# Optimization experiments

Hardware: AMD Instinct MI355X
Metric: run time of the kernel (lower is better)

## Reference

```python
import jax, jax.numpy as jnp
import numpy as np

IN_BW = 4
W_BW = 4
EPS = 1e-5


def quantize(x, bw):
    # k-bit uniform quantizer on [-1, 1 - 2^(1-bw)] with straight-through rounding
    scale = 2.0 ** (bw - 1)
    xc = jnp.clip(x, -1.0, 1.0 - 1.0 / scale)
    q = jnp.round(xc * scale) / scale
    return xc + jax.lax.stop_gradient(q - xc)


def bconv(x, w, stride):
    # BinarizeConv2d: quantize activations (in_bw) and weights (weight_bw), then conv
    return jax.lax.conv_general_dilated(
        quantize(x, IN_BW), quantize(w, W_BW),
        window_strides=stride, padding='VALID',
        dimension_numbers=('NCHW', 'OIHW', 'NCHW'))


def bn2d(x, g, b):
    mean = x.mean(axis=(0, 2, 3), keepdims=True)
    var = x.var(axis=(0, 2, 3), keepdims=True)
    return (x - mean) * jax.lax.rsqrt(var + EPS) * g.reshape(1, -1, 1, 1) + b.reshape(1, -1, 1, 1)


def bn1d(x, g, b):
    mean = x.mean(axis=0, keepdims=True)
    var = x.var(axis=0, keepdims=True)
    return (x - mean) * jax.lax.rsqrt(var + EPS) * g + b


def htanh(x):
    return jnp.clip(x, -1.0, 1.0)


def setup_inputs() -> dict:
    key = jax.random.key(0)
    ks = jax.random.split(key, 24)
    B = 8192
    d = {'x': jax.random.normal(ks[0], (B, 1, 1250, 1), dtype=jnp.float32)}
    # conv weights OIHW
    shapes = [(3, 1, 6, 1), (5, 3, 5, 1), (10, 5, 4, 1), (20, 10, 4, 1), (20, 20, 4, 1)]
    for i, s in enumerate(shapes):
        d[f'w{i+1}'] = 0.3 * jax.random.normal(ks[1 + i], s, dtype=jnp.float32)
    d['fw1'] = 0.3 * jax.random.normal(ks[6], (10, 740), dtype=jnp.float32)
    d['fw2'] = 0.3 * jax.random.normal(ks[7], (2, 10), dtype=jnp.float32)
    chans = [3, 5, 10, 20, 20, 10, 2]
    for i, c in enumerate(chans):
        d[f'g{i+1}'] = 1.0 + 0.1 * jax.random.normal(ks[8 + i], (c,), dtype=jnp.float32)
        d[f'b{i+1}'] = 0.1 * jax.random.normal(ks[15 + i], (c,), dtype=jnp.float32)
    return d


def reference(x, w1, w2, w3, w4, w5, fw1, fw2,
              g1, g2, g3, g4, g5, g6, g7,
              b1, b2, b3, b4, b5, b6, b7):
    h = htanh(bn2d(bconv(x, w1, (2, 1)), g1, b1))
    h = htanh(bn2d(bconv(h, w2, (2, 1)), g2, b2))
    h = htanh(bn2d(bconv(h, w3, (2, 1)), g3, b3))
    h = htanh(bn2d(bconv(h, w4, (2, 1)), g4, b4))
    h = htanh(bn2d(bconv(h, w5, (2, 1)), g5, b5))
    h = h.reshape(h.shape[0], -1)  # (B, 20*37*1) = (B, 740)
    # dropout is identity in eval mode
    h = htanh(bn1d(quantize(h, IN_BW) @ quantize(fw1, W_BW).T, g6, b6))
    h = bn1d(quantize(h, IN_BW) @ quantize(fw2, W_BW).T, g7, b7)
    return h
```

## Files before the change

kernel.cpp:

```cpp
#include <hip/hip_runtime.h>

#define DEV __device__ __forceinline__

DEV float qwt(float w) {
    float y = fminf(fmaxf(w, -1.0f), 0.875f);
    return rintf(y * 8.0f) * 0.125f;
}
DEV int qw8i(float w) {
    float y = fminf(fmaxf(w, -1.0f), 0.875f);
    return (int)rintf(y * 8.0f);
}
DEV int q8i(float x, float a, float b) {
    float y = fmaf(x, a, b);
    y = fminf(fmaxf(y, -1.0f), 0.875f);
    return (int)rintf(y * 8.0f);
}
DEV float qact(float x, float a, float b) {
    float y = fmaf(x, a, b);
    y = fminf(fmaxf(y, -1.0f), 0.875f);
    return rintf(y * 8.0f) * 0.125f;
}

DEV int dot4(int a, int b, int c) {
#if __has_builtin(__builtin_amdgcn_sdot4)
    return __builtin_amdgcn_sdot4(a, b, c, false);
#else
    c += (int)(signed char)(a)       * (int)(signed char)(b);
    c += (int)(signed char)(a >> 8)  * (int)(signed char)(b >> 8);
    c += (int)(signed char)(a >> 16) * (int)(signed char)(b >> 16);
    c += (int)(signed char)(a >> 24) * (int)(signed char)(b >> 24);
    return c;
#endif
}
DEV unsigned alignpair(unsigned hi, unsigned lo, int bits) {
#if __has_builtin(__builtin_amdgcn_alignbit)
    return __builtin_amdgcn_alignbit(hi, lo, bits);
#else
    return bits ? ((lo >> bits) | (hi << (32 - bits))) : lo;
#endif
}

DEV void pack_layer(const float* w, int* o, int CIN, int COUT, int K, int t) {
    int KW = (K + 3) / 4;
    for (int i = t; i < COUT * CIN * KW; i += 256) {
        int j = i % KW, cc = i / KW;
        unsigned r = 0;
        for (int u = 0; u < 4; u++) {
            int k = 4 * j + u;
            int b = (k < K) ? (qw8i(w[cc * K + k]) & 0xff) : 0;
            r |= (unsigned)b << (8 * u);
        }
        o[i] = (int)r;
    }
}
__global__ __launch_bounds__(256) void pack_k(
    const float* w1, const float* w2, const float* w3, const float* w4, const float* w5,
    int* o1, int* o2, int* o3, int* o4, int* o5)
{
    int t = threadIdx.x;
    pack_layer(w1, o1, 1, 3, 6, t);
    pack_layer(w2, o2, 3, 5, 5, t);
    pack_layer(w3, o3, 5, 10, 4, t);
    pack_layer(w4, o4, 10, 20, 4, t);
    pack_layer(w5, o5, 20, 20, 4, t);
}

template<int CIN,int COUT,int K,int LINP,int LOUT,int LOUTP,int P,int R,bool IN_FLOAT,int LIN=0>
__global__ __launch_bounds__(256) void conv_k(
    const void* __restrict__ in_, const int* __restrict__ wqi,
    const float* __restrict__ tr, short* __restrict__ out,
    float* __restrict__ partial, int B)
{
    constexpr int KW   = (K + 3) / 4;
    constexpr int NE   = P + 2 * KW - 2 + 1;
    constexpr int ND   = (2 * (NE - 1) + 3) / 4 + 2;
    constexpr int LO_P = (LOUT + P - 1) / P;
    constexpr int GROUPS = R * LO_P;

    __shared__ __align__(16) signed char smem[R * CIN * LINP + 32];
    __shared__ float ts[CIN > 0 ? CIN : 1], tb[CIN > 0 ? CIN : 1];
    __shared__ float red[4][2 * COUT];

    const int tid = threadIdx.x;

    if constexpr (!IN_FLOAT) {
        if (tid < CIN) {
            ts[tid] = tr[tid] * 0.015625f;
            tb[tid] = tr[CIN + tid];
        }
        __syncthreads();
    }

    const int r0   = blockIdx.x * R;
    const int rcnt = min(R, B - r0);

    if constexpr (IN_FLOAT) {
        constexpr int CH = LIN / 2;
        const float2* gp = (const float2*)in_;
        for (int c = tid; c < rcnt * CH; c += 256) {
            int r = c / CH, rem = c - r * CH;
            float2 v = gp[(size_t)(r0 + r) * CH + rem];
            int b0 = q8i(v.x, 1.f, 0.f) & 0xff;
            int b1 = q8i(v.y, 1.f, 0.f) & 0xff;
            *(unsigned short*)(smem + r * LINP + rem * 2) =
                (unsigned short)(b0 | (b1 << 8));
        }
    } else {
        constexpr int CH  = CIN * LINP / 8;
        constexpr int CHC = LINP / 8;
        const int4* gp = (const int4*)((const short*)in_ + (size_t)r0 * CIN * LINP);
        for (int c = tid; c < rcnt * CH; c += 256) {
            int rem = c % CH;
            int ci = rem / CHC;
            float a = ts[ci], bo = tb[ci];
            int4 v = gp[c];
            int vs[4] = { v.x, v.y, v.z, v.w };
            unsigned pk[2];
#pragma unroll
            for (int u = 0; u < 2; u++) {
                unsigned pp = 0;
#pragma unroll
                for (int j = 0; j < 2; j++) {
                    int word = vs[u * 2 + j];
                    int b0 = q8i((float)(short)(word & 0xffff), a, bo) & 0xff;
                    int b1 = q8i((float)(short)(word >> 16),    a, bo) & 0xff;
                    pp |= (unsigned)(b0 | (b1 << 8)) << (16 * j);
                }
                pk[u] = pp;
            }
            ((uint2*)smem)[c] = make_uint2(pk[0], pk[1]);
        }
    }
    __syncthreads();

    float tsum[COUT], tsq[COUT];
#pragma unroll
    for (int c = 0; c < COUT; c++) { tsum[c] = 0.f; tsq[c] = 0.f; }

#pragma unroll 1
    for (int g = tid; g < GROUPS; g += 256) {
        int r = g / LO_P;
        if (r >= rcnt) continue;
        int l0   = (g - r * LO_P) * P;
        int pact = min(P, LOUT - l0);

        int acc[COUT][P];
#pragma unroll
        for (int co = 0; co < COUT; co++)
#pragma unroll
            for (int p = 0; p < P; p++) acc[co][p] = 0;

        const int ibase = r * CIN * LINP + 2 * l0;
        const int sh    = (P % 2 == 0) ? 0 : (ibase & 3);

        for (int ci = 0; ci < CIN; ci++) {
            const int* sp = (const int*)smem + ((ci * LINP + (ibase & ~3)) >> 2);
            int d[ND];
#pragma unroll
            for (int j = 0; j < ND; j++) d[j] = sp[j];
            int e[NE];
#pragma unroll
            for (int i = 0; i < NE; i++) {
                int off = sh + 2 * i;
                e[i] = (int)alignpair((unsigned)d[off / 4 + 1], (unsigned)d[off / 4], (off & 3) * 8);
            }
#pragma unroll
            for (int co = 0; co < COUT; co++) {
#pragma unroll
                for (int j = 0; j < KW; j++) {
                    int wv = wqi[(co * CIN + ci) * KW + j];
#pragma unroll
                    for (int p = 0; p < P; p++)
                        acc[co][p] = dot4(e[p + 2 * j], wv, acc[co][p]);
                }
            }
        }

        const size_t ob = (size_t)(r0 + r) * COUT * LOUTP + l0;
#pragma unroll
        for (int co = 0; co < COUT; co++) {
            if (pact == P) {
                short tmp[P];
#pragma unroll
                for (int p = 0; p < P; p++) {
                    tmp[p] = (short)acc[co][p];
                    float v = (float)acc[co][p] * 0.015625f;
                    tsum[co] += v;
                    tsq[co]   = fmaf(v, v, tsq[co]);
                }
                short* op = &out[ob + (size_t)co * LOUTP];
                if constexpr (P == 1) {
                    op[0] = tmp[0];
                } else if constexpr (P == 2) {
                    *(short2*)op = make_short2(tmp[0], tmp[1]);
                } else if constexpr (P == 4) {
                    *(short4*)op = make_short4(tmp[0], tmp[1], tmp[2], tmp[3]);
                } else if constexpr (P == 8) {
                    *(short4*)op       = make_short4(tmp[0], tmp[1], tmp[2], tmp[3]);
                    *(short4*)(op + 4) = make_short4(tmp[4], tmp[5], tmp[6], tmp[7]);
                }
            } else {
#pragma unroll
                for (int p = 0; p < P; p++) {
                    if (p < pact) {
                        out[ob + (size_t)co * LOUTP + p] = (short)acc[co][p];
                        float v = (float)acc[co][p] * 0.015625f;
                        tsum[co] += v;
                        tsq[co]   = fmaf(v, v, tsq[co]);
                    }
                }
            }
        }
    }

    const int lane = tid & 63, wid = tid >> 6;
#pragma unroll
    for (int co = 0; co < COUT; co++) {
        float s = tsum[co], q = tsq[co];
        for (int off = 32; off > 0; off >>= 1) {
            s += __shfl_down(s, off, 64);
            q += __shfl_down(q, off, 64);
        }
        if (lane == 0) { red[wid][2 * co] = s; red[wid][2 * co + 1] = q; }
    }
    __syncthreads();
    if (tid < 2 * COUT) {
        float v = red[0][tid] + red[1][tid] + red[2][tid] + red[3][tid];
        partial[(size_t)blockIdx.x * (2 * COUT) + tid] = v;
    }
}

__global__ __launch_bounds__(256) void finalize_k(
    const float* __restrict__ partial, int G, int C, double N,
    const float* __restrict__ gamma, const float* __restrict__ beta,
    float* __restrict__ trout)
{
    const int c = blockIdx.x;
    double s = 0.0, q = 0.0;
    for (int g = threadIdx.x; g < G; g += 256) {
        s += (double)partial[(size_t)g * 2 * C + 2 * c];
        q += (double)partial[(size_t)g * 2 * C + 2 * c + 1];
    }
    for (int off = 32; off > 0; off >>= 1) {
        s += __shfl_down(s, off, 64);
        q += __shfl_down(q, off, 64);
    }
    __shared__ double rs[4], rq[4];
    int lane = threadIdx.x & 63, wid = threadIdx.x >> 6;
    if (lane == 0) { rs[wid] = s; rq[wid] = q; }
    __syncthreads();
    if (threadIdx.x == 0) {
        double S = rs[0] + rs[1] + rs[2] + rs[3];
        double Q = rq[0] + rq[1] + rq[2] + rq[3];
        double mean = S / N;
        double var  = Q / N - mean * mean;
        double inv  = 1.0 / sqrt(var + 1e-5);
        double sc   = (double)gamma[c] * inv;
        trout[c]     = (float)sc;
        trout[C + c] = (float)((double)beta[c] - mean * sc);
    }
}

__global__ __launch_bounds__(256) void fc1_k(
    const short* __restrict__ y5, const float* __restrict__ fw1,
    const float* __restrict__ tr, float* __restrict__ z1,
    float* __restrict__ partial, int B)
{
    __shared__ float wq[7400];
    __shared__ float ts[20], tb[20];
    __shared__ float red[4][20];
    const int tid = threadIdx.x;
    for (int i = tid; i < 7400; i += 256) wq[i] = qwt(fw1[i]);
    if (tid < 20) { ts[tid] = tr[tid]; tb[tid] = tr[20 + tid]; }
    __syncthreads();

    const int lane = tid & 63, wid = tid >> 6;
    float tsum[10], tsq[10];
#pragma unroll
    for (int j = 0; j < 10; j++) { tsum[j] = 0.f; tsq[j] = 0.f; }

#pragma unroll 1
    for (int r = blockIdx.x * 4 + wid; r < B; r += gridDim.x * 4) {
        const short* xr = y5 + (size_t)r * 800;
        float acc[10];
#pragma unroll
        for (int j = 0; j < 10; j++) acc[j] = 0.f;
#pragma unroll 1
        for (int f = lane; f < 740; f += 64) {
            int c = f / 37, pos = f - c * 37;
            float x = qact((float)xr[c * 40 + pos] * 0.015625f, ts[c], tb[c]);
#pragma unroll
            for (int j = 0; j < 10; j++) acc[j] = fmaf(x, wq[j * 740 + f], acc[j]);
        }
#pragma unroll
        for (int j = 0; j < 10; j++) {
            float v = acc[j];
            for (int off = 1; off < 64; off <<= 1) v += __shfl_xor(v, off, 64);
            tsum[j] += v; tsq[j] = fmaf(v, v, tsq[j]);
            if (lane == j) z1[(size_t)r * 10 + j] = v;
        }
    }
    if (lane == 0) {
#pragma unroll
        for (int j = 0; j < 10; j++) { red[wid][2 * j] = tsum[j]; red[wid][2 * j + 1] = tsq[j]; }
    }
    __syncthreads();
    if (tid < 20) {
        float v = red[0][tid] + red[1][tid] + red[2][tid] + red[3][tid];
        partial[(size_t)blockIdx.x * 20 + tid] = v;
    }
}

__global__ __launch_bounds__(256) void fc2_fused_k(
    const float* __restrict__ z1, const float* __restrict__ fw2,
    const float* __restrict__ part6, int G6,
    const float* __restrict__ g6, const float* __restrict__ b6,
    const float* __restrict__ g7, const float* __restrict__ b7,
    float* __restrict__ outp, int B)
{
    __shared__ float zbuf[16384];
    __shared__ double dred[4][20];
    __shared__ double dtot[20];
    __shared__ float ts7[10], tb7[10], wq2[20];
    __shared__ float fr[4][4];
    __shared__ float tr8[4];

    const int tid = threadIdx.x;
    const int lane = tid & 63, wid = tid >> 6;

    double ls[20];
#pragma unroll
    for (int c = 0; c < 20; c++) ls[c] = 0.0;
    for (int g = tid; g < G6; g += 256) {
#pragma unroll
        for (int c = 0; c < 20; c++) ls[c] += (double)part6[(size_t)g * 20 + c];
    }
#pragma unroll
    for (int c = 0; c < 20; c++) {
        double v = ls[c];
        for (int off = 32; off > 0; off >>= 1) v += __shfl_down(v, off, 64);
        if (lane == 0) dred[wid][c] = v;
    }
    if (tid < 20) wq2[tid] = qwt(fw2[tid]);
    __syncthreads();
    if (tid < 20) dtot[tid] = dred[0][tid] + dred[1][tid] + dred[2][tid] + dred[3][tid];
    __syncthreads();
    if (tid < 10) {
        double N = (double)B;
        double mean = dtot[2 * tid] / N;
        double var  = dtot[2 * tid + 1] / N - mean * mean;
        double inv  = 1.0 / sqrt(var + 1e-5);
        double sc   = (double)g6[tid] * inv;
        ts7[tid] = (float)sc;
        tb7[tid] = (float)((double)b6[tid] - mean * sc);
    }
    __syncthreads();

    float s0 = 0.f, q0 = 0.f, s1 = 0.f, q1 = 0.f;
#pragma unroll 1
    for (int r = tid; r < B; r += 256) {
        float a0 = 0.f, a1 = 0.f;
#pragma unroll
        for (int i = 0; i < 10; i++) {
            float x = qact(z1[(size_t)r * 10 + i], ts7[i], tb7[i]);
            a0 = fmaf(x, wq2[i], a0);
            a1 = fmaf(x, wq2[10 + i], a1);
        }
        zbuf[r * 2]     = a0;
        zbuf[r * 2 + 1] = a1;
        s0 += a0; q0 = fmaf(a0, a0, q0);
        s1 += a1; q1 = fmaf(a1, a1, q1);
    }
    for (int off = 32; off > 0; off >>= 1) {
        s0 += __shfl_down(s0, off, 64); q0 += __shfl_down(q0, off, 64);
        s1 += __shfl_down(s1, off, 64); q1 += __shfl_down(q1, off, 64);
    }
    if (lane == 0) { fr[wid][0] = s0; fr[wid][1] = q0; fr[wid][2] = s1; fr[wid][3] = q1; }
    __syncthreads();
    if (tid < 2) {
        double S = 0.0, Q = 0.0;
        for (int w = 0; w < 4; w++) { S += (double)fr[w][2 * tid]; Q += (double)fr[w][2 * tid + 1]; }
        double N = (double)B;
        double mean = S / N;
        double var  = Q / N - mean * mean;
        double inv  = 1.0 / sqrt(var + 1e-5);
        double sc   = (double)g7[tid] * inv;
        tr8[tid]     = (float)sc;
        tr8[2 + tid] = (float)((double)b7[tid] - mean * sc);
    }
    __syncthreads();
    for (int i = tid; i < 2 * B; i += 256) {
        int c = i & 1;
        outp[i] = fmaf(zbuf[i], tr8[c], tr8[2 + c]);
    }
}

extern "C" void kernel_launch(void* const* d_in, const int* in_sizes, int n_in,
                              void* d_out, int out_size, void* d_ws, size_t ws_size,
                              hipStream_t stream)
{
    const float* x   = (const float*)d_in[0];
    const float* w1  = (const float*)d_in[1];
    const float* w2  = (const float*)d_in[2];
    const float* w3  = (const float*)d_in[3];
    const float* w4  = (const float*)d_in[4];
    const float* w5  = (const float*)d_in[5];
    const float* fw1 = (const float*)d_in[6];
    const float* fw2 = (const float*)d_in[7];
    const float *g[7], *bb[7];
    for (int i = 0; i < 7; i++) { g[i] = (const float*)d_in[8 + 2 * i]; bb[i] = (const float*)d_in[9 + 2 * i]; }

    char* ws = (char*)d_ws;
    size_t off = 0;
    auto alloc = [&](size_t bytes) -> void* {
        void* p = ws + off;
        off += (bytes + 255) & ~(size_t)255;
        return p;
    };
    short* SA      = (short*)alloc((size_t)8192 * 3 * 624 * 2);
    short* SB      = (short*)alloc((size_t)8192 * 20 * 80 * 2);
    float* z1      = (float*)alloc((size_t)81920 * 4);
    float* partial = (float*)alloc((size_t)81920 * 4);
    int*   wp1 = (int*)alloc(64);   int* wp2 = (int*)alloc(256);
    int*   wp3 = (int*)alloc(256);  int* wp4 = (int*)alloc(1024);
    int*   wp5 = (int*)alloc(2048);
    float* tr2 = (float*)alloc(256); float* tr3 = (float*)alloc(256);
    float* tr4 = (float*)alloc(256); float* tr5 = (float*)alloc(256);
    float* tr6 = (float*)alloc(256);

    const int B = 8192;

    pack_k<<<1, 256, 0, stream>>>(w1, w2, w3, w4, w5, wp1, wp2, wp3, wp4, wp5);

    {
        int grid = (B + 2) / 3;
        conv_k<1, 3, 6, 1252, 623, 624, 8, 3, true, 1250>
            <<<grid, 256, 0, stream>>>(x, wp1, nullptr, SA, partial, B);
        finalize_k<<<3, 256, 0, stream>>>(partial, grid, 3, (double)B * 623.0, g[0], bb[0], tr2);
    }
    {
        int grid = (B + 5) / 6;
        conv_k<3, 5, 5, 624, 310, 312, 8, 6, false>
            <<<grid, 256, 0, stream>>>(SA, wp2, tr2, SB, partial, B);
        finalize_k<<<5, 256, 0, stream>>>(partial, grid, 5, (double)B * 310.0, g[1], bb[1], tr3);
    }
    {
        int grid = (B + 5) / 6;
        conv_k<5, 10, 4, 312, 154, 160, 4, 6, false>
            <<<grid, 256, 0, stream>>>(SB, wp3, tr3, SA, partial, B);
        finalize_k<<<10, 256, 0, stream>>>(partial, grid, 10, (double)B * 154.0, g[2], bb[2], tr4);
    }
    {
        int grid = (B + 6) / 7;
        conv_k<10, 20, 4, 160, 76, 80, 2, 7, false>
            <<<grid, 256, 0, stream>>>(SA, wp4, tr4, SB, partial, B);
        finalize_k<<<20, 256, 0, stream>>>(partial, grid, 20, (double)B * 76.0, g[3], bb[3], tr5);
    }
    {
        int grid = (B + 6) / 7;
        conv_k<20, 20, 4, 80, 37, 40, 1, 7, false>
            <<<grid, 256, 0, stream>>>(SB, wp5, tr5, SA, partial, B);
        finalize_k<<<20, 256, 0, stream>>>(partial, grid, 20, (double)B * 37.0, g[4], bb[4], tr6);
    }
    {
        int grid = 512;
        fc1_k<<<grid, 256, 0, stream>>>(SA, fw1, tr6, z1, partial, B);
    }
    fc2_fused_k<<<1, 256, 0, stream>>>(z1, fw2, partial, 512,
                                       g[5], bb[5], g[6], bb[6],
                                       (float*)d_out, B);
}
```

Before: 305.8 us.

## Fuse the whole network into one persistent cooperative kernel with grid syncs

Replaces the chain of per-layer conv, finalize, fc1 and fc2 kernels with a single cooperative persistent kernel. Layers are separated by grid.sync(), and each block recomputes the batch-norm scale and shift from the partial sums. Each block processes 16-row tiles in a grid-stride loop, and weight packing is done per block in LDS. This removes roughly a dozen kernel launches and the serial single-block tail, at the cost of grid-wide barriers, fixed occupancy limits (512 or 256 blocks) and redundant per-block reduction work.

```diff
diff --git a/kernel.cpp b/kernel.cpp
--- a/kernel.cpp
+++ b/kernel.cpp
@@ -1,4 +1,7 @@
 #include <hip/hip_runtime.h>
+#include <hip/hip_cooperative_groups.h>
+
+namespace cg = cooperative_groups;
 
 #define DEV __device__ __forceinline__
 
@@ -40,173 +43,187 @@
 #endif
 }
 
-DEV void pack_layer(const float* w, int* o, int CIN, int COUT, int K, int t) {
-    int KW = (K + 3) / 4;
-    for (int i = t; i < COUT * CIN * KW; i += 256) {
+struct Params {
+    const float* x;
+    const float* w1; const float* w2; const float* w3; const float* w4; const float* w5;
+    const float* fw1; const float* fw2;
+    const float* g[7]; const float* bb[7];
+    short* y1; short* y2; short* y3; short* y4; short* y5;
+    float* z1; float* z2;
+    float* part[7];
+    float* out;
+    int G;
+};
+
+template<int C>
+DEV void bridge(const float* part, int G, double N,
+                const float* gamma, const float* beta,
+                float* tsA, float* tbA, float fold, double* dsc)
+{
+    const int tid = threadIdx.x;
+    if (tid < 2 * C * 4) {
+        int slot = tid >> 2, ch = tid & 3;
+        double s = 0.0;
+        for (int g = ch; g < G; g += 4)
+            s += (double)part[(size_t)g * 2 * C + slot];
+        dsc[tid] = s;
+    }
+    __syncthreads();
+    if (tid < C) {
+        double S = dsc[8 * tid]     + dsc[8 * tid + 1] + dsc[8 * tid + 2] + dsc[8 * tid + 3];
+        double Q = dsc[8 * tid + 4] + dsc[8 * tid + 5] + dsc[8 * tid + 6] + dsc[8 * tid + 7];
+        double mean = S / N;
+        double var  = Q / N - mean * mean;
+        double inv  = 1.0 / sqrt(var + 1e-5);
+        double sc   = (double)gamma[tid] * inv;
+        tsA[tid] = (float)sc * fold;
+        tbA[tid] = (float)((double)beta[tid] - mean * sc);
+    }
+    __syncthreads();
+}
+
+template<int CIN,int COUT,int K,int LINP,int LOUT,int LOUTP,int P,bool IN_FLOAT,int LIN>
+DEV void conv_layer(const void* in_, const float* w, short* out, float* partial,
+                    int G, signed char* uni, int* wql,
+                    const float* tsA, const float* tbA, float (*redf)[40])
+{
+    constexpr int KW   = (K + 3) / 4;
+    constexpr int NE   = P + 2 * KW - 1;
+    constexpr int ND   = (2 * (NE - 1) + 3) / 4 + 2;
+    constexpr int LO_P = (LOUT + P - 1) / P;
+    constexpr int GROUPS = 16 * LO_P;
+
+    const int tid = threadIdx.x;
+    const int bid = blockIdx.x;
+
+    for (int i = tid; i < COUT * CIN * KW; i += 256) {
         int j = i % KW, cc = i / KW;
-        unsigned r = 0;
+        unsigned rr = 0;
         for (int u = 0; u < 4; u++) {
             int k = 4 * j + u;
-            int b = (k < K) ? (qw8i(w[cc * K + k]) & 0xff) : 0;
-            r |= (unsigned)b << (8 * u);
-        }
-        o[i] = (int)r;
-    }
-}
-__global__ __launch_bounds__(256) void pack_k(
-    const float* w1, const float* w2, const float* w3, const float* w4, const float* w5,
-    int* o1, int* o2, int* o3, int* o4, int* o5)
-{
-    int t = threadIdx.x;
-    pack_layer(w1, o1, 1, 3, 6, t);
-    pack_layer(w2, o2, 3, 5, 5, t);
-    pack_layer(w3, o3, 5, 10, 4, t);
-    pack_layer(w4, o4, 10, 20, 4, t);
-    pack_layer(w5, o5, 20, 20, 4, t);
-}
-
-template<int CIN,int COUT,int K,int LINP,int LOUT,int LOUTP,int P,int R,bool IN_FLOAT,int LIN=0>
-__global__ __launch_bounds__(256) void conv_k(
-    const void* __restrict__ in_, const int* __restrict__ wqi,
-    const float* __restrict__ tr, short* __restrict__ out,
-    float* __restrict__ partial, int B)
-{
-    constexpr int KW   = (K + 3) / 4;
-    constexpr int NE   = P + 2 * KW - 2 + 1;
-    constexpr int ND   = (2 * (NE - 1) + 3) / 4 + 2;
-    constexpr int LO_P = (LOUT + P - 1) / P;
-    constexpr int GROUPS = R * LO_P;
-
-    __shared__ __align__(16) signed char smem[R * CIN * LINP + 32];
-    __shared__ float ts[CIN > 0 ? CIN : 1], tb[CIN > 0 ? CIN : 1];
-    __shared__ float red[4][2 * COUT];
-
-    const int tid = threadIdx.x;
-
-    if constexpr (!IN_FLOAT) {
-        if (tid < CIN) {
-            ts[tid] = tr[tid] * 0.015625f;
-            tb[tid] = tr[CIN + tid];
-        }
+            int bv = (k < K) ? (qw8i(w[cc * K + k]) & 0xff) : 0;
+            rr |= (unsigned)bv << (8 * u);
+        }
+        wql[i] = (int)rr;
+    }
+
+    float tsum[COUT], tsq[COUT];
+#pragma unroll
+    for (int c = 0; c < COUT; c++) { tsum[c] = 0.f; tsq[c] = 0.f; }
+
+    for (int tile = bid; tile < 512; tile += G) {
+        const int r0 = tile * 16;
         __syncthreads();
-    }
-
-    const int r0   = blockIdx.x * R;
-    const int rcnt = min(R, B - r0);
-
-    if constexpr (IN_FLOAT) {
-        constexpr int CH = LIN / 2;
-        const float2* gp = (const float2*)in_;
-        for (int c = tid; c < rcnt * CH; c += 256) {
-            int r = c / CH, rem = c - r * CH;
-            float2 v = gp[(size_t)(r0 + r) * CH + rem];
-            int b0 = q8i(v.x, 1.f, 0.f) & 0xff;
-            int b1 = q8i(v.y, 1.f, 0.f) & 0xff;
-            *(unsigned short*)(smem + r * LINP + rem * 2) =
-                (unsigned short)(b0 | (b1 << 8));
-        }
-    } else {
-        constexpr int CH  = CIN * LINP / 8;
-        constexpr int CHC = LINP / 8;
-        const int4* gp = (const int4*)((const short*)in_ + (size_t)r0 * CIN * LINP);
-        for (int c = tid; c < rcnt * CH; c += 256) {
-            int rem = c % CH;
-            int ci = rem / CHC;
-            float a = ts[ci], bo = tb[ci];
-            int4 v = gp[c];
-            int vs[4] = { v.x, v.y, v.z, v.w };
-            unsigned pk[2];
-#pragma unroll
-            for (int u = 0; u < 2; u++) {
-                unsigned pp = 0;
-#pragma unroll
-                for (int j = 0; j < 2; j++) {
-                    int word = vs[u * 2 + j];
-                    int b0 = q8i((float)(short)(word & 0xffff), a, bo) & 0xff;
-                    int b1 = q8i((float)(short)(word >> 16),    a, bo) & 0xff;
-                    pp |= (unsigned)(b0 | (b1 << 8)) << (16 * j);
+
+        if constexpr (IN_FLOAT) {
+            constexpr int CH = LIN / 2;
+            const float2* gp = (const float2*)in_;
+            for (int c = tid; c < 16 * CH; c += 256) {
+                int r = c / CH, rem = c - r * CH;
+                float2 v = gp[(size_t)(r0 + r) * CH + rem];
+                int b0 = q8i(v.x, 1.f, 0.f) & 0xff;
+                int b1 = q8i(v.y, 1.f, 0.f) & 0xff;
+                *(unsigned short*)(uni + r * LINP + rem * 2) =
+                    (unsigned short)(b0 | (b1 << 8));
+            }
+        } else {
+            constexpr int CH  = CIN * LINP / 8;
+            constexpr int CHC = LINP / 8;
+            const int4* gp = (const int4*)((const short*)in_ + (size_t)r0 * CIN * LINP);
+            for (int c = tid; c < 16 * CH; c += 256) {
+                int rem = c % CH;
+                int ci = rem / CHC;
+                float a = tsA[ci], bo = tbA[ci];
+                int4 v = gp[c];
+                int vs[4] = { v.x, v.y, v.z, v.w };
+                unsigned pk[2];
+#pragma unroll
+                for (int u = 0; u < 2; u++) {
+                    unsigned pp = 0;
+#pragma unroll
+                    for (int j = 0; j < 2; j++) {
+                        int word = vs[u * 2 + j];
+                        int b0 = q8i((float)(short)(word & 0xffff), a, bo) & 0xff;
+                        int b1 = q8i((float)(short)(word >> 16),    a, bo) & 0xff;
+                        pp |= (unsigned)(b0 | (b1 << 8)) << (16 * j);
+                    }
+                    pk[u] = pp;
                 }
-                pk[u] = pp;
-            }
-            ((uint2*)smem)[c] = make_uint2(pk[0], pk[1]);
-        }
-    }
-    __syncthreads();
-
-    float tsum[COUT], tsq[COUT];
-#pragma unroll
-    for (int c = 0; c < COUT; c++) { tsum[c] = 0.f; tsq[c] = 0.f; }
+                ((uint2*)uni)[c] = make_uint2(pk[0], pk[1]);
+            }
+        }
+        __syncthreads();
 
 #pragma unroll 1
-    for (int g = tid; g < GROUPS; g += 256) {
-        int r = g / LO_P;
-        if (r >= rcnt) continue;
-        int l0   = (g - r * LO_P) * P;
-        int pact = min(P, LOUT - l0);
-
-        int acc[COUT][P];
-#pragma unroll
-        for (int co = 0; co < COUT; co++)
-#pragma unroll
-            for (int p = 0; p < P; p++) acc[co][p] = 0;
-
-        const int ibase = r * CIN * LINP + 2 * l0;
-        const int sh    = (P % 2 == 0) ? 0 : (ibase & 3);
-
-        for (int ci = 0; ci < CIN; ci++) {
-            const int* sp = (const int*)smem + ((ci * LINP + (ibase & ~3)) >> 2);
-            int d[ND];
-#pragma unroll
-            for (int j = 0; j < ND; j++) d[j] = sp[j];
-            int e[NE];
-#pragma unroll
-            for (int i = 0; i < NE; i++) {
-                int off = sh + 2 * i;
-                e[i] = (int)alignpair((unsigned)d[off / 4 + 1], (unsigned)d[off / 4], (off & 3) * 8);
-            }
+        for (int g = tid; g < GROUPS; g += 256) {
+            int r = g / LO_P;
+            int l0   = (g - r * LO_P) * P;
+            int pact = min(P, LOUT - l0);
+
+            int acc[COUT][P];
+#pragma unroll
+            for (int co = 0; co < COUT; co++)
+#pragma unroll
+                for (int p = 0; p < P; p++) acc[co][p] = 0;
+
+            const int ibase = r * CIN * LINP + 2 * l0;
+            const int sh    = (P % 2 == 0) ? 0 : (ibase & 3);
+
+            for (int ci = 0; ci < CIN; ci++) {
+                const int* sp = (const int*)uni + ((ci * LINP + (ibase & ~3)) >> 2);
+                int d[ND];
+#pragma unroll
+                for (int j = 0; j < ND; j++) d[j] = sp[j];
+                int e[NE];
+#pragma unroll
+                for (int i = 0; i < NE; i++) {
+                    int off = sh + 2 * i;
+                    e[i] = (int)alignpair((unsigned)d[off / 4 + 1], (unsigned)d[off / 4], (off & 3) * 8);
+                }
+#pragma unroll
+                for (int co = 0; co < COUT; co++) {
+#pragma unroll
+                    for (int j = 0; j < KW; j++) {
+                        int wv = wql[(co * CIN + ci) * KW + j];
+#pragma unroll
+                        for (int p = 0; p < P; p++)
+                            acc[co][p] = dot4(e[p + 2 * j], wv, acc[co][p]);
+                    }
+                }
+            }
+
+            const size_t ob = (size_t)(r0 + r) * COUT * LOUTP + l0;
 #pragma unroll
             for (int co = 0; co < COUT; co++) {
-#pragma unroll
-                for (int j = 0; j < KW; j++) {
-                    int wv = wqi[(co * CIN + ci) * KW + j];
-#pragma unroll
-                    for (int p = 0; p < P; p++)
-                        acc[co][p] = dot4(e[p + 2 * j], wv, acc[co][p]);
-                }
-            }
-        }
-
-        const size_t ob = (size_t)(r0 + r) * COUT * LOUTP + l0;
-#pragma unroll
-        for (int co = 0; co < COUT; co++) {
-            if (pact == P) {
-                short tmp[P];
-#pragma unroll
-                for (int p = 0; p < P; p++) {
-                    tmp[p] = (short)acc[co][p];
-                    float v = (float)acc[co][p] * 0.015625f;
-                    tsum[co] += v;
-                    tsq[co]   = fmaf(v, v, tsq[co]);
-                }
-                short* op = &out[ob + (size_t)co * LOUTP];
-                if constexpr (P == 1) {
-                    op[0] = tmp[0];
-                } else if constexpr (P == 2) {
-                    *(short2*)op = make_short2(tmp[0], tmp[1]);
-                } else if constexpr (P == 4) {
-                    *(short4*)op = make_short4(tmp[0], tmp[1], tmp[2], tmp[3]);
-                } else if constexpr (P == 8) {
-                    *(short4*)op       = make_short4(tmp[0], tmp[1], tmp[2], tmp[3]);
-                    *(short4*)(op + 4) = make_short4(tmp[4], tmp[5], tmp[6], tmp[7]);
-                }
-            } else {
-#pragma unroll
-                for (int p = 0; p < P; p++) {
-                    if (p < pact) {
-                        out[ob + (size_t)co * LOUTP + p] = (short)acc[co][p];
+                if (pact == P) {
+                    short tmp[P];
+#pragma unroll
+                    for (int p = 0; p < P; p++) {
+                        tmp[p] = (short)acc[co][p];
                         float v = (float)acc[co][p] * 0.015625f;
                         tsum[co] += v;
                         tsq[co]   = fmaf(v, v, tsq[co]);
+                    }
+                    short* op = &out[ob + (size_t)co * LOUTP];
+                    if constexpr (P == 1) {
+                        op[0] = tmp[0];
+                    } else if constexpr (P == 2) {
+                        *(short2*)op = make_short2(tmp[0], tmp[1]);
+                    } else if constexpr (P == 4) {
+                        *(short4*)op = make_short4(tmp[0], tmp[1], tmp[2], tmp[3]);
+                    } else if constexpr (P == 8) {
+                        *(short4*)op       = make_short4(tmp[0], tmp[1], tmp[2], tmp[3]);
+                        *(short4*)(op + 4) = make_short4(tmp[4], tmp[5], tmp[6], tmp[7]);
+                    }
+                } else {
+#pragma unroll
+                    for (int p = 0; p < P; p++) {
+                        if (p < pact) {
+                            out[ob + (size_t)co * LOUTP + p] = (short)acc[co][p];
+                            float v = (float)acc[co][p] * 0.015625f;
+                            tsum[co] += v;
+                            tsq[co]   = fmaf(v, v, tsq[co]);
+                        }
                     }
                 }
             }
@@ -221,252 +238,194 @@
             s += __shfl_down(s, off, 64);
             q += __shfl_down(q, off, 64);
         }
-        if (lane == 0) { red[wid][2 * co] = s; red[wid][2 * co + 1] = q; }
-    }
-    __syncthreads();
-    if (tid < 2 * COUT) {
-        float v = red[0][tid] + red[1][tid] + red[2][tid] + red[3][tid];
-        partial[(size_t)blockIdx.x * (2 * COUT) + tid] = v;
-    }
-}
-
-__global__ __launch_bounds__(256) void finalize_k(
-    const float* __restrict__ partial, int G, int C, double N,
-    const float* __restrict__ gamma, const float* __restrict__ beta,
-    float* __restrict__ trout)
-{
-    const int c = blockIdx.x;
-    double s = 0.0, q = 0.0;
-    for (int g = threadIdx.x; g < G; g += 256) {
-        s += (double)partial[(size_t)g * 2 * C + 2 * c];
-        q += (double)partial[(size_t)g * 2 * C + 2 * c + 1];
-    }
-    for (int off = 32; off > 0; off >>= 1) {
-        s += __shfl_down(s, off, 64);
-        q += __shfl_down(q, off, 64);
-    }
-    __shared__ double rs[4], rq[4];
-    int lane = threadIdx.x & 63, wid = threadIdx.x >> 6;
-    if (lane == 0) { rs[wid] = s; rq[wid] = q; }
-    __syncthreads();
-    if (threadIdx.x == 0) {
-        double S = rs[0] + rs[1] + rs[2] + rs[3];
-        double Q = rq[0] + rq[1] + rq[2] + rq[3];
-        double mean = S / N;
-        double var  = Q / N - mean * mean;
-        double inv  = 1.0 / sqrt(var + 1e-5);
-        double sc   = (double)gamma[c] * inv;
-        trout[c]     = (float)sc;
-        trout[C + c] = (float)((double)beta[c] - mean * sc);
-    }
-}
-
-__global__ __launch_bounds__(256) void fc1_k(
-    const short* __restrict__ y5, const float* __restrict__ fw1,
-    const float* __restrict__ tr, float* __restrict__ z1,
-    float* __restrict__ partial, int B)
-{
-    __shared__ float wq[7400];
-    __shared__ float ts[20], tb[20];
-    __shared__ float red[4][20];
-    const int tid = threadIdx.x;
-    for (int i = tid; i < 7400; i += 256) wq[i] = qwt(fw1[i]);
-    if (tid < 20) { ts[tid] = tr[tid]; tb[tid] = tr[20 + tid]; }
-    __syncthreads();
-
-    const int lane = tid & 63, wid = tid >> 6;
-    float tsum[10], tsq[10];
-#pragma unroll
-    for (int j = 0; j < 10; j++) { tsum[j] = 0.f; tsq[j] = 0.f; }
-
-#pragma unroll 1
-    for (int r = blockIdx.x * 4 + wid; r < B; r += gridDim.x * 4) {
-        const short* xr = y5 + (size_t)r * 800;
-        float acc[10];
-#pragma unroll
-        for (int j = 0; j < 10; j++) acc[j] = 0.f;
-#pragma unroll 1
-        for (int f = lane; f < 740; f += 64) {
-            int c = f / 37, pos = f - c * 37;
-            float x = qact((float)xr[c * 40 + pos] * 0.015625f, ts[c], tb[c]);
-#pragma unroll
-            for (int j = 0; j < 10; j++) acc[j] = fmaf(x, wq[j * 740 + f], acc[j]);
-        }
-#pragma unroll
-        for (int j = 0; j < 10; j++) {
-            float v = acc[j];
-            for (int off = 1; off < 64; off <<= 1) v += __shfl_xor(v, off, 64);
-            tsum[j] += v; tsq[j] = fmaf(v, v, tsq[j]);
-            if (lane == j) z1[(size_t)r * 10 + j] = v;
-        }
-    }
-    if (lane == 0) {
-#pragma unroll
-        for (int j = 0; j < 10; j++) { red[wid][2 * j] = tsum[j]; red[wid][2 * j + 1] = tsq[j]; }
-    }
-    __syncthreads();
-    if (tid < 20) {
-        float v = red[0][tid] + red[1][tid] + red[2][tid] + red[3][tid];
-        partial[(size_t)blockIdx.x * 20 + tid] = v;
-    }
-}
-
-__global__ __launch_bounds__(256) void fc2_fused_k(
-    const float* __restrict__ z1, const float* __restrict__ fw2,
-    const float* __restrict__ part6, int G6,
-    const float* __restrict__ g6, const float* __restrict__ b6,
-    const float* __restrict__ g7, const float* __restrict__ b7,
-    float* __restrict__ outp, int B)
-{
-    __shared__ float zbuf[16384];
-    __shared__ double dred[4][20];
-    __shared__ double dtot[20];
-    __shared__ float ts7[10], tb7[10], wq2[20];
-    __shared__ float fr[4][4];
-    __shared__ float tr8[4];
-
+        if (lane == 0) { redf[wid][2 * co] = s; redf[wid][2 * co + 1] = q; }
+    }
+    __syncthreads();
+    if (tid < 2 * COUT)
+        partial[(size_t)bid * (2 * COUT) + tid] =
+            redf[0][tid] + redf[1][tid] + redf[2][tid] + redf[3][tid];
+    __syncthreads();
+}
+
+DEV void fc1_layer(const short* y5, const float* fw1, float* z1, float* partial,
+                   int G, float* wqf, const float* tsA, const float* tbA,
+                   float (*redf)[40])
+{
     const int tid = threadIdx.x;
     const int lane = tid & 63, wid = tid >> 6;
 
-    double ls[20];
-#pragma unroll
-    for (int c = 0; c < 20; c++) ls[c] = 0.0;
-    for (int g = tid; g < G6; g += 256) {
-#pragma unroll
-        for (int c = 0; c < 20; c++) ls[c] += (double)part6[(size_t)g * 20 + c];
-    }
-#pragma unroll
-    for (int c = 0; c < 20; c++) {
-        double v = ls[c];
-        for (int off = 32; off > 0; off >>= 1) v += __shfl_down(v, off, 64);
-        if (lane == 0) dred[wid][c] = v;
-    }
-    if (tid < 20) wq2[tid] = qwt(fw2[tid]);
-    __syncthreads();
-    if (tid < 20) dtot[tid] = dred[0][tid] + dred[1][tid] + dred[2][tid] + dred[3][tid];
-    __syncthreads();
-    if (tid < 10) {
-        double N = (double)B;
-        double mean = dtot[2 * tid] / N;
-        double var  = dtot[2 * tid + 1] / N - mean * mean;
-        double inv  = 1.0 / sqrt(var + 1e-5);
-        double sc   = (double)g6[tid] * inv;
-        ts7[tid] = (float)sc;
-        tb7[tid] = (float)((double)b6[tid] - mean * sc);
-    }
+    for (int i = tid; i < 7400; i += 256) wqf[i] = qwt(fw1[i]);
+    __syncthreads();
+
+    float tsum[10], tsq[10];
+#pragma unroll
+    for (int j = 0; j < 10; j++) { tsum[j] = 0.f; tsq[j] = 0.f; }
+
+#pragma unroll 1
+    for (int tile = blockIdx.x; tile < 512; tile += G) {
+#pragma unroll 1
+        for (int pass = 0; pass < 4; pass++) {
+            int r = tile * 16 + pass * 4 + wid;
+            const short* xr = y5 + (size_t)r * 800;
+            float acc[10];
+#pragma unroll
+            for (int j = 0; j < 10; j++) acc[j] = 0.f;
+#pragma unroll 1
+            for (int f = lane; f < 740; f += 64) {
+                int c = f / 37, pos = f - c * 37;
+                float xv = qact((float)xr[c * 40 + pos] * 0.015625f, tsA[c], tbA[c]);
+#pragma unroll
+                for (int j = 0; j < 10; j++) acc[j] = fmaf(xv, wqf[j * 740 + f], acc[j]);
+            }
+#pragma unroll
+            for (int j = 0; j < 10; j++) {
+                float v = acc[j];
+                for (int off = 1; off < 64; off <<= 1) v += __shfl_xor(v, off, 64);
+                tsum[j] += v; tsq[j] = fmaf(v, v, tsq[j]);
+                if (lane == j) z1[(size_t)r * 10 + j] = v;
+            }
+        }
+    }
+    if (lane == 0) {
+#pragma unroll
+        for (int j = 0; j < 10; j++) { redf[wid][2 * j] = tsum[j]; redf[wid][2 * j + 1] = tsq[j]; }
+    }
+    __syncthreads();
+    if (tid < 20)
+        partial[(size_t)blockIdx.x * 20 + tid] =
+            redf[0][tid] + redf[1][tid] + redf[2][tid] + redf[3][tid];
+    __syncthreads();
+}
+
+DEV void fc2_layer(const float* z1, const float* fw2, float* z2, float* partial,
+                   int G, float* wq2l, const float* tsA, const float* tbA,
+                   float (*redf)[40])
+{
+    const int tid = threadIdx.x;
+    if (tid < 20) wq2l[tid] = qwt(fw2[tid]);
     __syncthreads();
 
     float s0 = 0.f, q0 = 0.f, s1 = 0.f, q1 = 0.f;
 #pragma unroll 1
-    for (int r = tid; r < B; r += 256) {
-        float a0 = 0.f, a1 = 0.f;
-#pragma unroll
-        for (int i = 0; i < 10; i++) {
-            float x = qact(z1[(size_t)r * 10 + i], ts7[i], tb7[i]);
-            a0 = fmaf(x, wq2[i], a0);
-            a1 = fmaf(x, wq2[10 + i], a1);
-        }
-        zbuf[r * 2]     = a0;
-        zbuf[r * 2 + 1] = a1;
-        s0 += a0; q0 = fmaf(a0, a0, q0);
-        s1 += a1; q1 = fmaf(a1, a1, q1);
-    }
+    for (int tile = blockIdx.x; tile < 512; tile += G) {
+        if (tid < 16) {
+            int r = tile * 16 + tid;
+            float a0 = 0.f, a1 = 0.f;
+#pragma unroll
+            for (int i = 0; i < 10; i++) {
+                float xv = qact(z1[(size_t)r * 10 + i], tsA[i], tbA[i]);
+                a0 = fmaf(xv, wq2l[i], a0);
+                a1 = fmaf(xv, wq2l[10 + i], a1);
+            }
+            z2[r * 2]     = a0;
+            z2[r * 2 + 1] = a1;
+            s0 += a0; q0 = fmaf(a0, a0, q0);
+            s1 += a1; q1 = fmaf(a1, a1, q1);
+        }
+    }
+    const int lane = tid & 63, wid = tid >> 6;
     for (int off = 32; off > 0; off >>= 1) {
         s0 += __shfl_down(s0, off, 64); q0 += __shfl_down(q0, off, 64);
         s1 += __shfl_down(s1, off, 64); q1 += __shfl_down(q1, off, 64);
     }
-    if (lane == 0) { fr[wid][0] = s0; fr[wid][1] = q0; fr[wid][2] = s1; fr[wid][3] = q1; }
-    __syncthreads();
-    if (tid < 2) {
-        double S = 0.0, Q = 0.0;
-        for (int w = 0; w < 4; w++) { S += (double)fr[w][2 * tid]; Q += (double)fr[w][2 * tid + 1]; }
-        double N = (double)B;
-        double mean = S / N;
-        double var  = Q / N - mean * mean;
-        double inv  = 1.0 / sqrt(var + 1e-5);
-        double sc   = (double)g7[tid] * inv;
-        tr8[tid]     = (float)sc;
-        tr8[2 + tid] = (float)((double)b7[tid] - mean * sc);
-    }
-    __syncthreads();
-    for (int i = tid; i < 2 * B; i += 256) {
-        int c = i & 1;
-        outp[i] = fmaf(zbuf[i], tr8[c], tr8[2 + c]);
-    }
+    if (lane == 0) { redf[wid][0] = s0; redf[wid][1] = q0; redf[wid][2] = s1; redf[wid][3] = q1; }
+    __syncthreads();
+    if (tid < 4)
+        partial[(size_t)blockIdx.x * 4 + tid] =
+            redf[0][tid] + redf[1][tid] + redf[2][tid] + redf[3][tid];
+    __syncthreads();
+}
+
+__global__ __launch_bounds__(256, 2) void net_k(Params p)
+{
+    __shared__ __align__(16) signed char uni[30080];
+    __shared__ __align__(16) int wql[400];
+    __shared__ float tsA[20], tbA[20];
+    __shared__ float redf[4][40];
+    __shared__ double dsc[160];
+    __shared__ float wq2l[20];
+
+    cg::grid_group grid = cg::this_grid();
+    const int G = p.G;
+
+    conv_layer<1, 3, 6, 1252, 623, 624, 8, true, 1250>(p.x,  p.w1, p.y1, p.part[0], G, uni, wql, tsA, tbA, redf);
+    grid.sync();
+    bridge<3>(p.part[0], G, 8192.0 * 623.0, p.g[0], p.bb[0], tsA, tbA, 0.015625f, dsc);
+
+    conv_layer<3, 5, 5, 624, 310, 312, 8, false, 0>(p.y1, p.w2, p.y2, p.part[1], G, uni, wql, tsA, tbA, redf);
+    grid.sync();
+    bridge<5>(p.part[1], G, 8192.0 * 310.0, p.g[1], p.bb[1], tsA, tbA, 0.015625f, dsc);
+
+    conv_layer<5, 10, 4, 312, 154, 160, 4, false, 0>(p.y2, p.w3, p.y3, p.part[2], G, uni, wql, tsA, tbA, redf);
+    grid.sync();
+    bridge<10>(p.part[2], G, 8192.0 * 154.0, p.g[2], p.bb[2], tsA, tbA, 0.015625f, dsc);
+
+    conv_layer<10, 20, 4, 160, 76, 80, 2, false, 0>(p.y3, p.w4, p.y4, p.part[3], G, uni, wql, tsA, tbA, redf);
+    grid.sync();
+    bridge<20>(p.part[3], G, 8192.0 * 76.0, p.g[3], p.bb[3], tsA, tbA, 0.015625f, dsc);
+
+    conv_layer<20, 20, 4, 80, 37, 40, 1, false, 0>(p.y4, p.w5, p.y5, p.part[4], G, uni, wql, tsA, tbA, redf);
+    grid.sync();
+    bridge<20>(p.part[4], G, 8192.0 * 37.0, p.g[4], p.bb[4], tsA, tbA, 1.0f, dsc);
+
+    fc1_layer(p.y5, p.fw1, p.z1, p.part[5], G, (float*)uni, tsA, tbA, redf);
+    grid.sync();
+    bridge<10>(p.part[5], G, 8192.0, p.g[5], p.bb[5], tsA, tbA, 1.0f, dsc);
+
+    fc2_layer(p.z1, p.fw2, p.z2, p.part[6], G, wq2l, tsA, tbA, redf);
+    grid.sync();
+    bridge<2>(p.part[6], G, 8192.0, p.g[6], p.bb[6], tsA, tbA, 1.0f, dsc);
+
+    for (int tile = blockIdx.x; tile < 512; tile += G)
+        for (int i = threadIdx.x; i < 32; i += 256) {
+            int idx = tile * 32 + i;
+            int c = idx & 1;
+            p.out[idx] = fmaf(p.z2[idx], tsA[c], tbA[c]);
+        }
 }
 
 extern "C" void kernel_launch(void* const* d_in, const int* in_sizes, int n_in,
                               void* d_out, int out_size, void* d_ws, size_t ws_size,
                               hipStream_t stream)
 {
-    const float* x   = (const float*)d_in[0];
-    const float* w1  = (const float*)d_in[1];
-    const float* w2  = (const float*)d_in[2];
-    const float* w3  = (const float*)d_in[3];
-    const float* w4  = (const float*)d_in[4];
-    const float* w5  = (const float*)d_in[5];
-    const float* fw1 = (const float*)d_in[6];
-    const float* fw2 = (const float*)d_in[7];
-    const float *g[7], *bb[7];
-    for (int i = 0; i < 7; i++) { g[i] = (const float*)d_in[8 + 2 * i]; bb[i] = (const float*)d_in[9 + 2 * i]; }
+    Params p;
+    p.x   = (const float*)d_in[0];
+    p.w1  = (const float*)d_in[1];
+    p.w2  = (const float*)d_in[2];
+    p.w3  = (const float*)d_in[3];
+    p.w4  = (const float*)d_in[4];
+    p.w5  = (const float*)d_in[5];
+    p.fw1 = (const float*)d_in[6];
+    p.fw2 = (const float*)d_in[7];
+    for (int i = 0; i < 7; i++) {
+        p.g[i]  = (const float*)d_in[8 + 2 * i];
+        p.bb[i] = (const float*)d_in[9 + 2 * i];
+    }
 
     char* ws = (char*)d_ws;
     size_t off = 0;
     auto alloc = [&](size_t bytes) -> void* {
-        void* p = ws + off;
+        void* q = ws + off;
         off += (bytes + 255) & ~(size_t)255;
-        return p;
+        return q;
     };
-    short* SA      = (short*)alloc((size_t)8192 * 3 * 624 * 2);
-    short* SB      = (short*)alloc((size_t)8192 * 20 * 80 * 2);
-    float* z1      = (float*)alloc((size_t)81920 * 4);
-    float* partial = (float*)alloc((size_t)81920 * 4);
-    int*   wp1 = (int*)alloc(64);   int* wp2 = (int*)alloc(256);
-    int*   wp3 = (int*)alloc(256);  int* wp4 = (int*)alloc(1024);
-    int*   wp5 = (int*)alloc(2048);
-    float* tr2 = (float*)alloc(256); float* tr3 = (float*)alloc(256);
-    float* tr4 = (float*)alloc(256); float* tr5 = (float*)alloc(256);
-    float* tr6 = (float*)alloc(256);
-
-    const int B = 8192;
-
-    pack_k<<<1, 256, 0, stream>>>(w1, w2, w3, w4, w5, wp1, wp2, wp3, wp4, wp5);
-
-    {
-        int grid = (B + 2) / 3;
-        conv_k<1, 3, 6, 1252, 623, 624, 8, 3, true, 1250>
-            <<<grid, 256, 0, stream>>>(x, wp1, nullptr, SA, partial, B);
-        finalize_k<<<3, 256, 0, stream>>>(partial, grid, 3, (double)B * 623.0, g[0], bb[0], tr2);
-    }
-    {
-        int grid = (B + 5) / 6;
-        conv_k<3, 5, 5, 624, 310, 312, 8, 6, false>
-            <<<grid, 256, 0, stream>>>(SA, wp2, tr2, SB, partial, B);
-        finalize_k<<<5, 256, 0, stream>>>(partial, grid, 5, (double)B * 310.0, g[1], bb[1], tr3);
-    }
-    {
-        int grid = (B + 5) / 6;
-        conv_k<5, 10, 4, 312, 154, 160, 4, 6, false>
-            <<<grid, 256, 0, stream>>>(SB, wp3, tr3, SA, partial, B);
-        finalize_k<<<10, 256, 0, stream>>>(partial, grid, 10, (double)B * 154.0, g[2], bb[2], tr4);
-    }
-    {
-        int grid = (B + 6) / 7;
-        conv_k<10, 20, 4, 160, 76, 80, 2, 7, false>
-            <<<grid, 256, 0, stream>>>(SA, wp4, tr4, SB, partial, B);
-        finalize_k<<<20, 256, 0, stream>>>(partial, grid, 20, (double)B * 76.0, g[3], bb[3], tr5);
-    }
-    {
-        int grid = (B + 6) / 7;
-        conv_k<20, 20, 4, 80, 37, 40, 1, 7, false>
-            <<<grid, 256, 0, stream>>>(SB, wp5, tr5, SA, partial, B);
-        finalize_k<<<20, 256, 0, stream>>>(partial, grid, 20, (double)B * 37.0, g[4], bb[4], tr6);
-    }
-    {
-        int grid = 512;
-        fc1_k<<<grid, 256, 0, stream>>>(SA, fw1, tr6, z1, partial, B);
-    }
-    fc2_fused_k<<<1, 256, 0, stream>>>(z1, fw2, partial, 512,
-                                       g[5], bb[5], g[6], bb[6],
-                                       (float*)d_out, B);
-}
+    p.y1 = (short*)alloc((size_t)8192 * 3 * 624 * 2);
+    p.y2 = (short*)alloc((size_t)8192 * 5 * 312 * 2);
+    p.y3 = (short*)alloc((size_t)8192 * 10 * 160 * 2);
+    p.y4 = (short*)alloc((size_t)8192 * 20 * 80 * 2);
+    p.y5 = (short*)alloc((size_t)8192 * 20 * 40 * 2);
+    p.z1 = (float*)alloc((size_t)81920 * 4);
+    p.z2 = (float*)alloc((size_t)16384 * 4);
+    const int pc[7] = { 6, 10, 20, 40, 40, 20, 4 };
+    for (int i = 0; i < 7; i++) p.part[i] = (float*)alloc((size_t)512 * pc[i] * 4);
+    p.out = (float*)d_out;
+
+    int maxB = 0;
+    if (hipOccupancyMaxActiveBlocksPerMultiprocessor(&maxB, net_k, 256, 0) != hipSuccess || maxB < 1)
+        maxB = 1;
+    int G = (maxB >= 2) ? 512 : 256;
+    p.G = G;
+
+    void* kargs[] = { (void*)&p };
+    hipLaunchCooperativeKernel((const void*)net_k, dim3(G), dim3(256), kargs, 0, stream);
+}
```

After: 793.8 us. 2.6x slower.
